# Performance work log

Measured on AMD Instinct MI355X. Metric: run time of the kernel, lower is better.

## Reference

```python
import jax, jax.numpy as jnp
import numpy as np

NUM_HEADS = 12


def setup_inputs() -> dict:
    key = jax.random.key(0)
    k1, k2, k3 = jax.random.split(key, 3)
    B, F, P, D = 8, 16, 196, 768
    x = jax.random.normal(k1, (B, F, P, D), dtype=jnp.float32)
    w_qkv = jax.random.normal(k2, (3 * D, D), dtype=jnp.float32) * (D ** -0.5)
    w_proj = jax.random.normal(k3, (D, D), dtype=jnp.float32) * (D ** -0.5)
    b_proj = jnp.zeros((D,), dtype=jnp.float32)
    return {"x": x, "w_qkv": w_qkv, "w_proj": w_proj, "b_proj": b_proj}


def reference(x, w_qkv, w_proj, b_proj):
    B, F, P, D = x.shape
    H = NUM_HEADS
    hd = D // H
    H2 = H // 2
    scale = hd ** -0.5
    N = F * P

    xf = x.reshape(B, N, D)
    qkv = jnp.einsum('bnd,ed->bne', xf, w_qkv)              # (B, N, 3D)
    qkv = qkv.reshape(B, N, 3, H, hd).transpose(2, 0, 3, 1, 4)
    q, k, v = qkv[0], qkv[1], qkv[2]                         # (B, H, N, hd)

    # split heads: first half spatial, second half temporal
    qs, qt = q[:, :H2], q[:, H2:]
    ks, kt = k[:, :H2], k[:, H2:]
    vs, vt = v[:, :H2], v[:, H2:]

    # spatial attention over patches within each frame
    qs = qs.reshape(B * F, H2, P, hd)
    ks = ks.reshape(B * F, H2, P, hd)
    vs = vs.reshape(B * F, H2, P, hd)
    attn_s = jax.nn.softmax(jnp.einsum('nhqd,nhkd->nhqk', qs, ks) * scale, axis=-1)
    ws = jnp.einsum('nhqk,nhkd->nhqd', attn_s, vs)           # (B*F, H2, P, hd)

    # temporal attention: raw row-major reshape, faithful to torch .reshape
    qt = qt.reshape(B * P, H2, F, hd)
    kt = kt.reshape(B * P, H2, F, hd)
    vt = vt.reshape(B * P, H2, F, hd)
    attn_t = jax.nn.softmax(jnp.einsum('mhqd,mhkd->mhqk', qt, kt) * scale, axis=-1)
    wt = jnp.einsum('mhqk,mhkd->mhqd', attn_t, vt)           # (B*P, H2, F, hd)

    ws = ws.reshape(B, H2, N, hd)
    wt = wt.reshape(B, H2, N, hd)
    w = jnp.concatenate([ws, wt], axis=1)                    # (B, H, N, hd)
    w = w.transpose(0, 2, 1, 3).reshape(B, N, D)

    out = jnp.einsum('bnd,ed->bne', w, w_proj) + b_proj
    return out.reshape(B, F, P, D)
```

## Files before the change

kernel.cpp:

```cpp
#include <hip/hip_runtime.h>

#define DEV __device__ __forceinline__

typedef _Float16 half8  __attribute__((ext_vector_type(8)));
typedef _Float16 half4h __attribute__((ext_vector_type(4)));
typedef float    f32x4  __attribute__((ext_vector_type(4)));

static constexpr int Bb = 8;
static constexpr int Ff = 16;
static constexpr int Pp = 196;
static constexpr int Dd = 768;
static constexpr int Hh = 12;
static constexpr int HD = 64;
static constexpr int Nn = 3136;
static constexpr int NC = 392;

#define MFMA(a, b, c) __builtin_amdgcn_mfma_f32_16x16x32_f16(a, b, c, 0, 0, 0)

DEV void gll16(const _Float16* g, _Float16* l) {
  __builtin_amdgcn_global_load_lds(
      (__attribute__((address_space(1))) void*)(g),
      (__attribute__((address_space(3))) void*)(l), 16, 0, 0);
}

DEV void lds_fence() { asm volatile("s_waitcnt lgkmcnt(0)" ::: "memory"); }

__global__ __launch_bounds__(256) void cvt_all(const float* __restrict__ x,
                                               const float* __restrict__ wq,
                                               const float* __restrict__ wp,
                                               _Float16* __restrict__ xh,
                                               _Float16* __restrict__ wqh,
                                               _Float16* __restrict__ wph) {
  const int NX = 4816896, NQ = 442368;
  int i = blockIdx.x * 256 + threadIdx.x;
  const float* s;
  _Float16* d;
  int j;
  if (i < NX) { s = x; d = xh; j = i; }
  else if (i < NX + NQ) { s = wq; d = wqh; j = i - NX; }
  else { s = wp; d = wph; j = i - NX - NQ; }
  f32x4 v = ((const f32x4*)s)[j];
  half4h h;
  h.x = (_Float16)v.x; h.y = (_Float16)v.y;
  h.z = (_Float16)v.z; h.w = (_Float16)v.w;
  ((half4h*)d)[j] = h;
}

__global__ __launch_bounds__(512, 1) void gemm_qkv(const _Float16* __restrict__ X,
                                                   const _Float16* __restrict__ W,
                                                   _Float16* __restrict__ Q8,
                                                   _Float16* __restrict__ K8,
                                                   _Float16* __restrict__ V8) {
  __shared__ __align__(16) _Float16 smem[4 * 16384];
  const int tid = threadIdx.x;
  const int lane = tid & 63, wid = tid >> 6;
  const int l15 = lane & 15, quad = lane >> 4;
  const int L = blockIdx.x;
  const int xcd = L & 7, idx = L >> 3;
  const int v = xcd * 110 + (xcd < 2 ? xcd : 2) + idx;
  const int bx = v % 9, by = v / 9;
  const int row0 = by * 256;
  const int e0 = bx * 256;
  const int wm = (wid >> 2) * 128, wn = (wid & 3) * 64;

  const _Float16* Ag = X + (size_t)row0 * Dd;
  const _Float16* Bg = W + (size_t)e0 * Dd;

  f32x4 acc[8][4];
#pragma unroll
  for (int i = 0; i < 8; ++i)
#pragma unroll
    for (int j = 0; j < 4; ++j) acc[i][j] = (f32x4)0.0f;

  const int c0 = tid, c1 = tid + 512;
  const int r0s = c0 >> 2, o0 = ((c0 & 3) ^ ((r0s >> 1) & 3)) * 8;
  const int r1s = c1 >> 2, o1 = ((c1 & 3) ^ ((r1s >> 1) & 3)) * 8;
  const int csel = (quad ^ ((l15 >> 1) & 3)) * 8;

  auto stage = [&](int t) {
    const int kn = t * 32;
    _Float16* An = smem + (t & 3) * 16384;
    _Float16* Bn = An + 8192;
    gll16(Ag + (size_t)r0s * Dd + kn + o0, An + c0 * 8);
    gll16(Ag + (size_t)r1s * Dd + kn + o1, An + c1 * 8);
    gll16(Bg + (size_t)r0s * Dd + kn + o0, Bn + c0 * 8);
    gll16(Bg + (size_t)r1s * Dd + kn + o1, Bn + c1 * 8);
  };

  stage(0);
  stage(1);
  stage(2);
  asm volatile("s_waitcnt vmcnt(8)" ::: "memory");
  asm volatile("s_barrier" ::: "memory");

  auto tile = [&](int T, int SL, bool STG, int WV) {
    if (STG) stage(T + 3);
    const _Float16* As_ = smem + SL * 16384;
    const _Float16* Bs_ = As_ + 8192;
    half8 af[8], bf[4];
#pragma unroll
    for (int m = 0; m < 8; ++m)
      af[m] = *(const half8*)(As_ + (wm + m * 16 + l15) * 32 + csel);
#pragma unroll
    for (int n = 0; n < 4; ++n)
      bf[n] = *(const half8*)(Bs_ + (wn + n * 16 + l15) * 32 + csel);
    __builtin_amdgcn_s_setprio(1);
#pragma unroll
    for (int m = 0; m < 8; ++m)
#pragma unroll
      for (int n = 0; n < 4; ++n) acc[m][n] = MFMA(af[m], bf[n], acc[m][n]);
    __builtin_amdgcn_s_setprio(0);
    if (WV == 8)      asm volatile("s_waitcnt vmcnt(8)" ::: "memory");
    else if (WV == 4) asm volatile("s_waitcnt vmcnt(4)" ::: "memory");
    else if (WV == 0) asm volatile("s_waitcnt vmcnt(0)" ::: "memory");
    if (WV >= 0) asm volatile("s_barrier" ::: "memory");
  };

#pragma unroll
  for (int g = 0; g < 6; ++g) {
#pragma unroll
    for (int u = 0; u < 4; ++u) {
      const int T = g * 4 + u;
      tile(T, u, T < 21, T < 21 ? 8 : (T == 21 ? 4 : (T == 22 ? 0 : -1)));
    }
  }

  __syncthreads();
  const int tsel = e0 / Dd;
  const int eb = e0 - tsel * Dd;
  if (tsel == 2) {
    for (int hf = 0; hf < 2; ++hf) {
      if ((wid >> 2) == hf) {
#pragma unroll
        for (int i = 0; i < 8; ++i)
#pragma unroll
          for (int j = 0; j < 4; ++j) {
            half4h hv;
#pragma unroll
            for (int r = 0; r < 4; ++r) hv[r] = (_Float16)acc[i][j][r];
            *(half4h*)(smem + (wn + j * 16 + l15) * 136 + i * 16 + quad * 4) = hv;
          }
      }
      __syncthreads();
#pragma unroll
      for (int z = 0; z < 8; ++z) {
        const int c = tid + z * 512;
        const int e = c >> 4, mc = c & 15;
        const half8 vv = *(const half8*)(smem + e * 136 + mc * 8);
        const int rg = row0 + hf * 128 + mc * 8;
        const int b = rg / Nn, n = rg % Nn;
        const int eg = eb + e;
        const int hh = eg >> 6, d = eg & 63;
        *(half8*)(V8 + (((size_t)(b * Hh + hh) * NC + (n >> 3)) * 64 + d) * 8) = vv;
      }
      __syncthreads();
    }
  } else {
    _Float16* Ob = (tsel == 0) ? Q8 : K8;
    for (int hf = 0; hf < 2; ++hf) {
      if ((wid >> 2) == hf) {
#pragma unroll
        for (int i = 0; i < 8; ++i)
#pragma unroll
          for (int j = 0; j < 4; ++j)
#pragma unroll
            for (int r = 0; r < 4; ++r)
              smem[(i * 16 + quad * 4 + r) * 264 + wn + j * 16 + l15] =
                  (_Float16)acc[i][j][r];
      }
      __syncthreads();
#pragma unroll
      for (int z = 0; z < 8; ++z) {
        const int c = tid + z * 512;
        const int m = c >> 5, ec = c & 31;
        const half8 vv = *(const half8*)(smem + m * 264 + ec * 8);
        const int rg = row0 + hf * 128 + m;
        const int b = rg / Nn, n = rg % Nn;
        const int eg = eb + ec * 8;
        const int hh = eg >> 6, dc = (eg >> 3) & 7;
        *(half8*)(Ob + (((size_t)(b * Hh + hh) * 8 + dc) * Nn + n) * 8) = vv;
      }
      __syncthreads();
    }
  }
}

__global__ __launch_bounds__(256) void gemm_proj(const _Float16* __restrict__ Wbuf,
                                                 const _Float16* __restrict__ Wp,
                                                 const float* __restrict__ bias,
                                                 float* __restrict__ Out) {
  __shared__ __align__(16) _Float16 smem[128 * 64];
  _Float16* As = smem;
  _Float16* Bs = smem + 128 * 32;
  const int tid = threadIdx.x;
  const int lane = tid & 63, wid = tid >> 6;
  const int l15 = lane & 15, quad = lane >> 4;
  const int L = blockIdx.x;
  const int v = (L & 7) * 147 + (L >> 3);
  const int bx = v % 6, by = v / 6;
  const int row0 = by * 128;
  const int e0 = bx * 128;
  const int wm = (wid >> 1) * 64, wn = (wid & 1) * 64;

  const _Float16* Ag = Wbuf + (size_t)row0 * Dd;
  const _Float16* Bg = Wp + (size_t)e0 * Dd;

  f32x4 acc[4][4];
#pragma unroll
  for (int i = 0; i < 4; ++i)
#pragma unroll
    for (int j = 0; j < 4; ++j) acc[i][j] = (f32x4)0.0f;

  const int c0 = tid, c1 = tid + 256;
  const int r0s = c0 >> 2, o0 = ((c0 & 3) ^ ((r0s >> 1) & 3)) * 8;
  const int r1s = c1 >> 2, o1 = ((c1 & 3) ^ ((r1s >> 1) & 3)) * 8;
  const int csel = ((quad ^ ((l15 >> 1) & 3))) * 8;

  for (int kt = 0; kt < 24; ++kt) {
    const int k0 = kt * 32;
    __syncthreads();
    gll16(Ag + (size_t)r0s * Dd + k0 + o0, As + c0 * 8);
    gll16(Bg + (size_t)r0s * Dd + k0 + o0, Bs + c0 * 8);
    gll16(Ag + (size_t)r1s * Dd + k0 + o1, As + c1 * 8);
    gll16(Bg + (size_t)r1s * Dd + k0 + o1, Bs + c1 * 8);
    __syncthreads();
    half8 af[4], bf[4];
#pragma unroll
    for (int t = 0; t < 4; ++t) {
      af[t] = *(const half8*)(As + (wm + t * 16 + l15) * 32 + csel);
      bf[t] = *(const half8*)(Bs + (wn + t * 16 + l15) * 32 + csel);
    }
#pragma unroll
    for (int i = 0; i < 4; ++i)
#pragma unroll
      for (int j = 0; j < 4; ++j) acc[i][j] = MFMA(af[i], bf[j], acc[i][j]);
  }

#pragma unroll
  for (int j = 0; j < 4; ++j) {
    const int e = e0 + wn + j * 16 + l15;
    const float bj = bias[e];
#pragma unroll
    for (int i = 0; i < 4; ++i) {
      const int rb = row0 + wm + i * 16 + quad * 4;
#pragma unroll
      for (int r = 0; r < 4; ++r)
        Out[(size_t)(rb + r) * Dd + e] = acc[i][j][r] + bj;
    }
  }
}

__global__ __launch_bounds__(256) void attn_spatial(const _Float16* __restrict__ Q8,
                                                    const _Float16* __restrict__ K8,
                                                    const _Float16* __restrict__ V8,
                                                    _Float16* __restrict__ Wbuf) {
  __shared__ __align__(16) _Float16 Vs[64 * 216];
  __shared__ __align__(16) _Float16 Plds[4][16 * 232];
  const int tid = threadIdx.x;
  const int lane = tid & 63, wid = tid >> 6;
  const int l15 = lane & 15, quad = lane >> 4;
  const int gid = blockIdx.x;
  const int h = gid % 6, f = (gid / 6) % Ff, b = gid / 96;
  const size_t bh = (size_t)b * Hh + h;
  const int g0 = f * Pp;
  const int off = g0 & 7;
  const int nc0 = g0 >> 3;
  const _Float16* Qp = Q8 + bh * 8 * (size_t)Nn * 8;
  const _Float16* Kp = K8 + bh * 8 * (size_t)Nn * 8;

  for (int c = tid; c < 26 * 64; c += 256) {
    const int d = c & 63, ncl = c >> 6;
    const half8 v = *(const half8*)(V8 + ((bh * NC + nc0 + ncl) * 64 + d) * 8);
    _Float16* dst = Vs + d * 216 + (8 - off) + ncl * 8;
    half4h lo, hi;
#pragma unroll
    for (int z = 0; z < 4; ++z) { lo[z] = v[z]; hi[z] = v[4 + z]; }
    *(half4h*)dst = lo;
    *(half4h*)(dst + 4) = hi;
  }
  _Float16* Pw = &Plds[wid][0];
  if (quad < 3) {
    half8 z8;
#pragma unroll
    for (int z = 0; z < 8; ++z) z8[z] = (_Float16)0.0f;
    *(half8*)(Pw + l15 * 232 + 208 + quad * 8) = z8;
  }
  __syncthreads();

  half8 h8z;
#pragma unroll
  for (int z = 0; z < 8; ++z) h8z[z] = (_Float16)0.0f;

  for (int it = 0; it < 4; ++it) {
    const int qi = wid + it * 4;
    if (qi > 12) continue;
    const int qr = qi * 16 + l15;
    const int qtok = g0 + (qr < 195 ? qr : 195);
    const half8 bq0 = *(const half8*)(Qp + ((size_t)quad * Nn + qtok) * 8);
    const half8 bq1 = *(const half8*)(Qp + ((size_t)(quad + 4) * Nn + qtok) * 8);

    f32x4 ex[13];
    float rs = 0.0f;
#pragma unroll
    for (int kt = 0; kt < 13; ++kt) {
      const int krr = kt * 16 + l15;
      const int ktok = g0 + (krr < 195 ? krr : 195);
      const half8 ak0 = *(const half8*)(Kp + ((size_t)quad * Nn + ktok) * 8);
      const half8 ak1 = *(const half8*)(Kp + ((size_t)(quad + 4) * Nn + ktok) * 8);
      f32x4 t = (f32x4)0.0f;
      t = MFMA(ak0, bq0, t);
      t = MFMA(ak1, bq1, t);
      f32x4 e;
#pragma unroll
      for (int r = 0; r < 4; ++r) e[r] = __expf(t[r] * 0.125f);
      if (kt == 12 && quad >= 1) e = (f32x4)0.0f;
      ex[kt] = e;
      rs += e[0] + e[1] + e[2] + e[3];
    }
#pragma unroll
    for (int kt = 0; kt < 13; ++kt)
#pragma unroll
      for (int r = 0; r < 4; ++r)
        Pw[l15 * 232 + kt * 16 + quad * 4 + r] = (_Float16)ex[kt][r];
    rs += __shfl_xor(rs, 16);
    rs += __shfl_xor(rs, 32);
    lds_fence();

    f32x4 acc[4];
#pragma unroll
    for (int mt = 0; mt < 4; ++mt) acc[mt] = (f32x4)0.0f;
#pragma unroll
    for (int c = 0; c < 7; ++c) {
      const half8 bp = *(const half8*)(Pw + l15 * 232 + c * 32 + quad * 8);
      const int k0 = c * 32 + quad * 8;
#pragma unroll
      for (int mt = 0; mt < 4; ++mt) {
        const int d = mt * 16 + l15;
        half8 av = h8z;
        if (k0 < 196) av = *(const half8*)(Vs + d * 216 + 8 + k0);
        acc[mt] = MFMA(av, bp, acc[mt]);
      }
    }
    const float inv = 1.0f / rs;
    if (qr < 196) {
      _Float16* base = Wbuf + (size_t)(b * Nn + g0 + qr) * Dd + h * HD;
#pragma unroll
      for (int mt = 0; mt < 4; ++mt) {
        half4h o;
#pragma unroll
        for (int r = 0; r < 4; ++r) o[r] = (_Float16)(acc[mt][r] * inv);
        *(half4h*)(base + mt * 16 + quad * 4) = o;
      }
    }
    __builtin_amdgcn_sched_barrier(0);
  }
}

__global__ __launch_bounds__(256) void attn_temporal(const _Float16* __restrict__ Q8,
                                                     const _Float16* __restrict__ K8,
                                                     const _Float16* __restrict__ V8,
                                                     _Float16* __restrict__ Wbuf) {
  __shared__ __align__(16) _Float16 Plds[4][16 * 40];
  const int tid = threadIdx.x;
  const int lane = tid & 63, wid = tid >> 6;
  const int l15 = lane & 15, quad = lane >> 4;
  const int p = blockIdx.x * 4 + wid;
  const int J0 = p << 4;
  const int b = J0 / 18816;
  const int rem = J0 % 18816;
  const int hh = rem / Nn;
  const int n0 = rem % Nn;
  const size_t bh = (size_t)b * Hh + 6 + hh;
  const _Float16* Qp = Q8 + bh * 8 * (size_t)Nn * 8;
  const _Float16* Kp = K8 + bh * 8 * (size_t)Nn * 8;
  _Float16* Pw = &Plds[wid][0];

  const int tok = n0 + l15;
  const half8 bq0 = *(const half8*)(Qp + ((size_t)quad * Nn + tok) * 8);
  const half8 bq1 = *(const half8*)(Qp + ((size_t)(quad + 4) * Nn + tok) * 8);
  const half8 ak0 = *(const half8*)(Kp + ((size_t)quad * Nn + tok) * 8);
  const half8 ak1 = *(const half8*)(Kp + ((size_t)(quad + 4) * Nn + tok) * 8);
  f32x4 t = (f32x4)0.0f;
  t = MFMA(ak0, bq0, t);
  t = MFMA(ak1, bq1, t);
  f32x4 e;
#pragma unroll
  for (int r = 0; r < 4; ++r) e[r] = __expf(t[r] * 0.125f);
  float rs = e[0] + e[1] + e[2] + e[3];
  rs += __shfl_xor(rs, 16);
  rs += __shfl_xor(rs, 32);

#pragma unroll
  for (int r = 0; r < 4; ++r) Pw[l15 * 40 + quad * 4 + r] = (_Float16)e[r];
  {
    half4h z4;
    z4.x = z4.y = z4.z = z4.w = (_Float16)0.0f;
    *(half4h*)(Pw + l15 * 40 + 16 + quad * 4) = z4;
  }
  lds_fence();

  const half8 bp = *(const half8*)(Pw + l15 * 40 + quad * 8);
  half8 h8z;
#pragma unroll
  for (int z = 0; z < 8; ++z) h8z[z] = (_Float16)0.0f;

  const float inv = 1.0f / rs;
  _Float16* base = Wbuf + (size_t)(b * Nn + n0 + l15) * Dd + (6 + hh) * HD;
#pragma unroll
  for (int mt = 0; mt < 4; ++mt) {
    const int d = mt * 16 + l15;
    half8 av = h8z;
    if (quad < 2)
      av = *(const half8*)(V8 + ((bh * NC + (n0 >> 3) + quad) * 64 + d) * 8);
    f32x4 acc = (f32x4)0.0f;
    acc = MFMA(av, bp, acc);
    half4h o;
#pragma unroll
    for (int r = 0; r < 4; ++r) o[r] = (_Float16)(acc[r] * inv);
    *(half4h*)(base + mt * 16 + quad * 4) = o;
  }
}

extern "C" void kernel_launch(void* const* d_in, const int* in_sizes, int n_in,
                              void* d_out, int out_size, void* d_ws, size_t ws_size,
                              hipStream_t stream) {
  const float* x = (const float*)d_in[0];
  const float* w_qkv = (const float*)d_in[1];
  const float* w_proj = (const float*)d_in[2];
  const float* b_proj = (const float*)d_in[3];
  float* out = (float*)d_out;

  _Float16* Xh = (_Float16*)d_ws;
  _Float16* Q8 = Xh + 19267584;
  _Float16* K8 = Q8 + 19267584;
  _Float16* V8 = K8 + 19267584;
  _Float16* Wqh = V8 + 19267584;
  _Float16* Wph = Wqh + 1769472;

  cvt_all<<<21120, 256, 0, stream>>>(x, w_qkv, w_proj, Xh, Wqh, Wph);
  gemm_qkv<<<882, 512, 0, stream>>>(Xh, Wqh, Q8, K8, V8);
  attn_spatial<<<768, 256, 0, stream>>>(Q8, K8, V8, Xh);
  attn_temporal<<<2352, 256, 0, stream>>>(Q8, K8, V8, Xh);
  gemm_proj<<<1176, 256, 0, stream>>>(Xh, Wph, b_proj, out);
}
```

Baseline: 382.8 us.

## Retile QKV and projection GEMMs to 128x256 with triple-buffered async pipeline

```diff
diff --git a/kernel.cpp b/kernel.cpp
--- a/kernel.cpp
+++ b/kernel.cpp
@@ -46,198 +46,213 @@
   ((half4h*)d)[j] = h;
 }
 
-__global__ __launch_bounds__(512, 1) void gemm_qkv(const _Float16* __restrict__ X,
+__global__ __launch_bounds__(256, 2) void gemm_qkv(const _Float16* __restrict__ X,
                                                    const _Float16* __restrict__ W,
                                                    _Float16* __restrict__ Q8,
                                                    _Float16* __restrict__ K8,
                                                    _Float16* __restrict__ V8) {
-  __shared__ __align__(16) _Float16 smem[4 * 16384];
+  __shared__ __align__(16) _Float16 smem[3 * 12288];
   const int tid = threadIdx.x;
   const int lane = tid & 63, wid = tid >> 6;
   const int l15 = lane & 15, quad = lane >> 4;
   const int L = blockIdx.x;
   const int xcd = L & 7, idx = L >> 3;
-  const int v = xcd * 110 + (xcd < 2 ? xcd : 2) + idx;
+  const int v = (xcd < 4 ? xcd * 221 : 884 + (xcd - 4) * 220) + idx;
   const int bx = v % 9, by = v / 9;
-  const int row0 = by * 256;
+  const int row0 = by * 128;
   const int e0 = bx * 256;
-  const int wm = (wid >> 2) * 128, wn = (wid & 3) * 64;
+  const int wm = (wid >> 1) * 64, wn = (wid & 1) * 128;
 
   const _Float16* Ag = X + (size_t)row0 * Dd;
   const _Float16* Bg = W + (size_t)e0 * Dd;
 
-  f32x4 acc[8][4];
-#pragma unroll
-  for (int i = 0; i < 8; ++i)
-#pragma unroll
-    for (int j = 0; j < 4; ++j) acc[i][j] = (f32x4)0.0f;
-
-  const int c0 = tid, c1 = tid + 512;
-  const int r0s = c0 >> 2, o0 = ((c0 & 3) ^ ((r0s >> 1) & 3)) * 8;
-  const int r1s = c1 >> 2, o1 = ((c1 & 3) ^ ((r1s >> 1) & 3)) * 8;
+  f32x4 acc[4][8];
+#pragma unroll
+  for (int i = 0; i < 4; ++i)
+#pragma unroll
+    for (int j = 0; j < 8; ++j) acc[i][j] = (f32x4)0.0f;
+
   const int csel = (quad ^ ((l15 >> 1) & 3)) * 8;
 
   auto stage = [&](int t) {
     const int kn = t * 32;
-    _Float16* An = smem + (t & 3) * 16384;
-    _Float16* Bn = An + 8192;
-    gll16(Ag + (size_t)r0s * Dd + kn + o0, An + c0 * 8);
-    gll16(Ag + (size_t)r1s * Dd + kn + o1, An + c1 * 8);
-    gll16(Bg + (size_t)r0s * Dd + kn + o0, Bn + c0 * 8);
-    gll16(Bg + (size_t)r1s * Dd + kn + o1, Bn + c1 * 8);
+    _Float16* base = smem + (t % 3) * 12288;
+#pragma unroll
+    for (int j = 0; j < 6; ++j) {
+      const int c = tid + j * 256;
+      const int r = c >> 2;
+      const int o = ((c & 3) ^ ((r >> 1) & 3)) * 8;
+      const _Float16* src = (j < 2) ? (Ag + (size_t)r * Dd + kn + o)
+                                    : (Bg + (size_t)(r - 128) * Dd + kn + o);
+      gll16(src, base + c * 8);
+    }
   };
 
   stage(0);
   stage(1);
-  stage(2);
-  asm volatile("s_waitcnt vmcnt(8)" ::: "memory");
+  asm volatile("s_waitcnt vmcnt(6)" ::: "memory");
   asm volatile("s_barrier" ::: "memory");
 
   auto tile = [&](int T, int SL, bool STG, int WV) {
-    if (STG) stage(T + 3);
-    const _Float16* As_ = smem + SL * 16384;
-    const _Float16* Bs_ = As_ + 8192;
-    half8 af[8], bf[4];
-#pragma unroll
-    for (int m = 0; m < 8; ++m)
+    if (STG) stage(T + 2);
+    const _Float16* As_ = smem + SL * 12288;
+    const _Float16* Bs_ = As_ + 4096;
+    half8 af[4], bf[8];
+#pragma unroll
+    for (int m = 0; m < 4; ++m)
       af[m] = *(const half8*)(As_ + (wm + m * 16 + l15) * 32 + csel);
 #pragma unroll
-    for (int n = 0; n < 4; ++n)
+    for (int n = 0; n < 8; ++n)
       bf[n] = *(const half8*)(Bs_ + (wn + n * 16 + l15) * 32 + csel);
+    if (WV == 6)      asm volatile("s_waitcnt vmcnt(6) lgkmcnt(0)" ::: "memory");
+    else if (WV == 0) asm volatile("s_waitcnt vmcnt(0) lgkmcnt(0)" ::: "memory");
+    else              asm volatile("s_waitcnt lgkmcnt(0)" ::: "memory");
+    asm volatile("s_barrier" ::: "memory");
     __builtin_amdgcn_s_setprio(1);
 #pragma unroll
-    for (int m = 0; m < 8; ++m)
-#pragma unroll
-      for (int n = 0; n < 4; ++n) acc[m][n] = MFMA(af[m], bf[n], acc[m][n]);
+    for (int m = 0; m < 4; ++m)
+#pragma unroll
+      for (int n = 0; n < 8; ++n) acc[m][n] = MFMA(af[m], bf[n], acc[m][n]);
     __builtin_amdgcn_s_setprio(0);
-    if (WV == 8)      asm volatile("s_waitcnt vmcnt(8)" ::: "memory");
-    else if (WV == 4) asm volatile("s_waitcnt vmcnt(4)" ::: "memory");
-    else if (WV == 0) asm volatile("s_waitcnt vmcnt(0)" ::: "memory");
-    if (WV >= 0) asm volatile("s_barrier" ::: "memory");
   };
 
 #pragma unroll
-  for (int g = 0; g < 6; ++g) {
-#pragma unroll
-    for (int u = 0; u < 4; ++u) {
-      const int T = g * 4 + u;
-      tile(T, u, T < 21, T < 21 ? 8 : (T == 21 ? 4 : (T == 22 ? 0 : -1)));
-    }
+  for (int g = 0; g < 8; ++g) {
+    const int T = 3 * g;
+    tile(T,     0, T < 22,     (T < 22) ? 6 : 0);
+    tile(T + 1, 1, T + 1 < 22, (T + 1 < 22) ? 6 : ((T + 1 == 22) ? 0 : -1));
+    tile(T + 2, 2, T + 2 < 22, (T + 2 < 22) ? 6 : ((T + 2 == 22) ? 0 : -1));
   }
 
   __syncthreads();
-  const int tsel = e0 / Dd;
+  const int tsel = bx / 3;
   const int eb = e0 - tsel * Dd;
   if (tsel == 2) {
-    for (int hf = 0; hf < 2; ++hf) {
-      if ((wid >> 2) == hf) {
-#pragma unroll
-        for (int i = 0; i < 8; ++i)
-#pragma unroll
-          for (int j = 0; j < 4; ++j) {
-            half4h hv;
-#pragma unroll
-            for (int r = 0; r < 4; ++r) hv[r] = (_Float16)acc[i][j][r];
-            *(half4h*)(smem + (wn + j * 16 + l15) * 136 + i * 16 + quad * 4) = hv;
-          }
+#pragma unroll
+    for (int i = 0; i < 4; ++i)
+#pragma unroll
+      for (int j = 0; j < 8; ++j) {
+        half4h hv;
+#pragma unroll
+        for (int r = 0; r < 4; ++r) hv[r] = (_Float16)acc[i][j][r];
+        *(half4h*)(smem + (wn + j * 16 + l15) * 132 + wm + i * 16 + quad * 4) = hv;
       }
-      __syncthreads();
-#pragma unroll
-      for (int z = 0; z < 8; ++z) {
-        const int c = tid + z * 512;
-        const int e = c >> 4, mc = c & 15;
-        const half8 vv = *(const half8*)(smem + e * 136 + mc * 8);
-        const int rg = row0 + hf * 128 + mc * 8;
-        const int b = rg / Nn, n = rg % Nn;
-        const int eg = eb + e;
-        const int hh = eg >> 6, d = eg & 63;
-        *(half8*)(V8 + (((size_t)(b * Hh + hh) * NC + (n >> 3)) * 64 + d) * 8) = vv;
-      }
-      __syncthreads();
+    __syncthreads();
+#pragma unroll
+    for (int z = 0; z < 16; ++z) {
+      const int c = tid + z * 256;
+      const int e = c >> 4, mc = c & 15;
+      const half8 vv = *(const half8*)(smem + e * 132 + mc * 8);
+      const int rg = row0 + mc * 8;
+      const int b = rg / Nn, n = rg % Nn;
+      const int em = eb + e;
+      const int hh = em >> 6, d = em & 63;
+      *(half8*)(V8 + (((size_t)(b * Hh + hh) * NC + (n >> 3)) * 64 + d) * 8) = vv;
     }
   } else {
     _Float16* Ob = (tsel == 0) ? Q8 : K8;
-    for (int hf = 0; hf < 2; ++hf) {
-      if ((wid >> 2) == hf) {
-#pragma unroll
-        for (int i = 0; i < 8; ++i)
-#pragma unroll
-          for (int j = 0; j < 4; ++j)
-#pragma unroll
-            for (int r = 0; r < 4; ++r)
-              smem[(i * 16 + quad * 4 + r) * 264 + wn + j * 16 + l15] =
-                  (_Float16)acc[i][j][r];
-      }
-      __syncthreads();
-#pragma unroll
-      for (int z = 0; z < 8; ++z) {
-        const int c = tid + z * 512;
-        const int m = c >> 5, ec = c & 31;
-        const half8 vv = *(const half8*)(smem + m * 264 + ec * 8);
-        const int rg = row0 + hf * 128 + m;
-        const int b = rg / Nn, n = rg % Nn;
-        const int eg = eb + ec * 8;
-        const int hh = eg >> 6, dc = (eg >> 3) & 7;
-        *(half8*)(Ob + (((size_t)(b * Hh + hh) * 8 + dc) * Nn + n) * 8) = vv;
-      }
-      __syncthreads();
-    }
-  }
-}
-
-__global__ __launch_bounds__(256) void gemm_proj(const _Float16* __restrict__ Wbuf,
-                                                 const _Float16* __restrict__ Wp,
-                                                 const float* __restrict__ bias,
-                                                 float* __restrict__ Out) {
-  __shared__ __align__(16) _Float16 smem[128 * 64];
-  _Float16* As = smem;
-  _Float16* Bs = smem + 128 * 32;
+#pragma unroll
+    for (int i = 0; i < 4; ++i)
+#pragma unroll
+      for (int j = 0; j < 8; ++j)
+#pragma unroll
+        for (int r = 0; r < 4; ++r)
+          smem[(wm + i * 16 + quad * 4 + r) * 264 + wn + j * 16 + l15] =
+              (_Float16)acc[i][j][r];
+    __syncthreads();
+#pragma unroll
+    for (int z = 0; z < 16; ++z) {
+      const int c = tid + z * 256;
+      const int ec = c >> 7, m = c & 127;
+      const half8 vv = *(const half8*)(smem + m * 264 + ec * 8);
+      const int rg = row0 + m;
+      const int b = rg / Nn, n = rg % Nn;
+      const int em = eb + ec * 8;
+      const int hh = em >> 6, dc = (em >> 3) & 7;
+      *(half8*)(Ob + (((size_t)(b * Hh + hh) * 8 + dc) * Nn + n) * 8) = vv;
+    }
+  }
+}
+
+__global__ __launch_bounds__(256, 2) void gemm_proj(const _Float16* __restrict__ Wbuf,
+                                                    const _Float16* __restrict__ Wp,
+                                                    const float* __restrict__ bias,
+                                                    float* __restrict__ Out) {
+  __shared__ __align__(16) _Float16 smem[3 * 12288];
   const int tid = threadIdx.x;
   const int lane = tid & 63, wid = tid >> 6;
   const int l15 = lane & 15, quad = lane >> 4;
   const int L = blockIdx.x;
-  const int v = (L & 7) * 147 + (L >> 3);
-  const int bx = v % 6, by = v / 6;
+  const int xcd = L & 7, idx = L >> 3;
+  const int v = (xcd < 4 ? xcd * 74 : 296 + (xcd - 4) * 73) + idx;
+  const int bx = v % 3, by = v / 3;
   const int row0 = by * 128;
-  const int e0 = bx * 128;
-  const int wm = (wid >> 1) * 64, wn = (wid & 1) * 64;
+  const int e0 = bx * 256;
+  const int wm = (wid >> 1) * 64, wn = (wid & 1) * 128;
 
   const _Float16* Ag = Wbuf + (size_t)row0 * Dd;
   const _Float16* Bg = Wp + (size_t)e0 * Dd;
 
-  f32x4 acc[4][4];
+  f32x4 acc[4][8];
 #pragma unroll
   for (int i = 0; i < 4; ++i)
 #pragma unroll
-    for (int j = 0; j < 4; ++j) acc[i][j] = (f32x4)0.0f;
-
-  const int c0 = tid, c1 = tid + 256;
-  const int r0s = c0 >> 2, o0 = ((c0 & 3) ^ ((r0s >> 1) & 3)) * 8;
-  const int r1s = c1 >> 2, o1 = ((c1 & 3) ^ ((r1s >> 1) & 3)) * 8;
-  const int csel = ((quad ^ ((l15 >> 1) & 3))) * 8;
-
-  for (int kt = 0; kt < 24; ++kt) {
-    const int k0 = kt * 32;
-    __syncthreads();
-    gll16(Ag + (size_t)r0s * Dd + k0 + o0, As + c0 * 8);
-    gll16(Bg + (size_t)r0s * Dd + k0 + o0, Bs + c0 * 8);
-    gll16(Ag + (size_t)r1s * Dd + k0 + o1, As + c1 * 8);
-    gll16(Bg + (size_t)r1s * Dd + k0 + o1, Bs + c1 * 8);
-    __syncthreads();
-    half8 af[4], bf[4];
-#pragma unroll
-    for (int t = 0; t < 4; ++t) {
-      af[t] = *(const half8*)(As + (wm + t * 16 + l15) * 32 + csel);
-      bf[t] = *(const half8*)(Bs + (wn + t * 16 + l15) * 32 + csel);
-    }
-#pragma unroll
-    for (int i = 0; i < 4; ++i)
-#pragma unroll
-      for (int j = 0; j < 4; ++j) acc[i][j] = MFMA(af[i], bf[j], acc[i][j]);
-  }
-
-#pragma unroll
-  for (int j = 0; j < 4; ++j) {
+    for (int j = 0; j < 8; ++j) acc[i][j] = (f32x4)0.0f;
+
+  const int csel = (quad ^ ((l15 >> 1) & 3)) * 8;
+
+  auto stage = [&](int t) {
+    const int kn = t * 32;
+    _Float16* base = smem + (t % 3) * 12288;
+#pragma unroll
+    for (int j = 0; j < 6; ++j) {
+      const int c = tid + j * 256;
+      const int r = c >> 2;
+      const int o = ((c & 3) ^ ((r >> 1) & 3)) * 8;
+      const _Float16* src = (j < 2) ? (Ag + (size_t)r * Dd + kn + o)
+                                    : (Bg + (size_t)(r - 128) * Dd + kn + o);
+      gll16(src, base + c * 8);
+    }
+  };
+
+  stage(0);
+  stage(1);
+  asm volatile("s_waitcnt vmcnt(6)" ::: "memory");
+  asm volatile("s_barrier" ::: "memory");
+
+  auto tile = [&](int T, int SL, bool STG, int WV) {
+    if (STG) stage(T + 2);
+    const _Float16* As_ = smem + SL * 12288;
+    const _Float16* Bs_ = As_ + 4096;
+    half8 af[4], bf[8];
+#pragma unroll
+    for (int m = 0; m < 4; ++m)
+      af[m] = *(const half8*)(As_ + (wm + m * 16 + l15) * 32 + csel);
+#pragma unroll
+    for (int n = 0; n < 8; ++n)
+      bf[n] = *(const half8*)(Bs_ + (wn + n * 16 + l15) * 32 + csel);
+    if (WV == 6)      asm volatile("s_waitcnt vmcnt(6) lgkmcnt(0)" ::: "memory");
+    else if (WV == 0) asm volatile("s_waitcnt vmcnt(0) lgkmcnt(0)" ::: "memory");
+    else              asm volatile("s_waitcnt lgkmcnt(0)" ::: "memory");
+    asm volatile("s_barrier" ::: "memory");
+    __builtin_amdgcn_s_setprio(1);
+#pragma unroll
+    for (int m = 0; m < 4; ++m)
+#pragma unroll
+      for (int n = 0; n < 8; ++n) acc[m][n] = MFMA(af[m], bf[n], acc[m][n]);
+    __builtin_amdgcn_s_setprio(0);
+  };
+
+#pragma unroll
+  for (int g = 0; g < 8; ++g) {
+    const int T = 3 * g;
+    tile(T,     0, T < 22,     (T < 22) ? 6 : 0);
+    tile(T + 1, 1, T + 1 < 22, (T + 1 < 22) ? 6 : ((T + 1 == 22) ? 0 : -1));
+    tile(T + 2, 2, T + 2 < 22, (T + 2 < 22) ? 6 : ((T + 2 == 22) ? 0 : -1));
+  }
+
+#pragma unroll
+  for (int j = 0; j < 8; ++j) {
     const int e = e0 + wn + j * 16 + l15;
     const float bj = bias[e];
 #pragma unroll
@@ -438,8 +453,8 @@
   _Float16* Wph = Wqh + 1769472;
 
   cvt_all<<<21120, 256, 0, stream>>>(x, w_qkv, w_proj, Xh, Wqh, Wph);
-  gemm_qkv<<<882, 512, 0, stream>>>(Xh, Wqh, Q8, K8, V8);
+  gemm_qkv<<<1764, 256, 0, stream>>>(Xh, Wqh, Q8, K8, V8);
   attn_spatial<<<768, 256, 0, stream>>>(Q8, K8, V8, Xh);
   attn_temporal<<<2352, 256, 0, stream>>>(Q8, K8, V8, Xh);
-  gemm_proj<<<1176, 256, 0, stream>>>(Xh, Wph, b_proj, out);
-}
+  gemm_proj<<<588, 256, 0, stream>>>(Xh, Wph, b_proj, out);
+}
```

After: 332.1 us. 1.15x faster.
